# Optimization experiments

Hardware: AMD Instinct MI355X
Metric: run time of the kernel (lower is better)

## Reference

```python
import jax, jax.numpy as jnp
import numpy as np

B = 131072   # number of graphs (ranked lists)
G = 128      # candidates per graph
TEMPERATURE = 1.0

def setup_inputs() -> dict:
    key = jax.random.key(0)
    k1, k2 = jax.random.split(key)
    scores = jax.random.normal(k1, (B * G,), dtype=jnp.float32)
    labels = jax.random.randint(k2, (B * G,), 0, 2, dtype=jnp.int32)  # binary relevance
    batch = jnp.repeat(jnp.arange(B, dtype=jnp.int32), G)             # segment ids, sorted
    return {"scores": scores, "labels": labels, "batch": batch}

def reference(scores, labels, batch):
    # batch encodes B contiguous equal-size segments of length G; reshape replaces
    # the original per-graph Python loop with one vectorized pass.
    s = scores.reshape(B, G) / TEMPERATURE            # [B, G]
    l = labels.reshape(B, G).astype(s.dtype)          # [B, G]
    probs = jax.nn.softmax(s, axis=1)
    pos = jnp.arange(1, G + 1, dtype=s.dtype)
    disc = 1.0 / jnp.log2(pos + 1.0)                  # [G]
    expected_dcg = jnp.sum(probs * l * disc, axis=1)  # [B]
    sorted_l = -jnp.sort(-l, axis=1)                  # descending sort of labels
    idcg = jnp.sum(sorted_l * disc, axis=1)           # [B]
    valid = idcg > 0                                  # graphs with labels.sum()==0 contribute loss 0
    ndcg = expected_dcg / jnp.where(valid, idcg, 1.0)
    loss_g = jnp.where(valid, 1.0 - ndcg, 0.0)
    # original counts every non-NaN graph, including zero-label graphs -> divide by B
    return jnp.sum(loss_g) / B
```

## Files before the change

### kernel.cpp

```cpp
#include <hip/hip_runtime.h>
#include <math.h>


#define G 128

__global__ void build_cumdisc_kernel(float* __restrict__ cumdisc) {
    int t = threadIdx.x;
    if (t <= G) {
        float s = 0.0f;
        for (int p = 1; p <= t; ++p) {
            s += 1.0f / log2f((float)(p + 1));
        }
        cumdisc[t] = s;
    }
}

__global__ __launch_bounds__(256) void ndcg_main_kernel(
        const float* __restrict__ scores,
        const int*   __restrict__ labels,
        const float* __restrict__ cumdisc,
        float*       __restrict__ partials,
        int nquads) {
    const int lane = threadIdx.x & 63;
    const int li   = lane & 15;
    const int gs   = lane >> 4;
    const int waveInBlock = threadIdx.x >> 6;
    const int gwave  = blockIdx.x * (blockDim.x >> 6) + waveInBlock;
    const int nwaves = gridDim.x * (blockDim.x >> 6);

    float d[8];
#pragma unroll
    for (int j = 0; j < 8; ++j) {
        int p = li * 8 + j;
        d[j] = 1.0f / log2f((float)(p + 2));
    }

    float acc = 0.0f;
    for (int q = gwave; q < nquads; q += nwaves) {
        const long long g = (long long)q * 4 + gs;
        const float4* sp = (const float4*)(scores + g * G + li * 8);
        const int4*   lp = (const int4*)(labels + g * G + li * 8);
        float4 sA = sp[0], sB = sp[1];
        int4   lA = lp[0], lB = lp[1];

        float s[8] = {sA.x, sA.y, sA.z, sA.w, sB.x, sB.y, sB.z, sB.w};
        int   l[8] = {lA.x, lA.y, lA.z, lA.w, lB.x, lB.y, lB.z, lB.w};

        float esum = 0.0f, num = 0.0f;
        int cnt = 0;
#pragma unroll
        for (int j = 0; j < 8; ++j) {
            float e = __expf(s[j]);
            esum += e;
            num  += e * d[j] * (float)l[j];
            cnt  += l[j];
        }

        float cntf = (float)cnt;
#pragma unroll
        for (int m = 1; m <= 8; m <<= 1) {
            esum += __shfl_xor(esum, m, 64);
            num  += __shfl_xor(num,  m, 64);
            cntf += __shfl_xor(cntf, m, 64);
        }
        int c = (int)cntf;
        float idcg = cumdisc[c];
        float loss = (c > 0) ? (1.0f - num / (esum * idcg)) : 0.0f;
        if (li == 0) acc += loss;
    }

    __shared__ float red[256];
    red[threadIdx.x] = acc;
    __syncthreads();
    for (int s2 = 128; s2 > 0; s2 >>= 1) {
        if (threadIdx.x < s2) red[threadIdx.x] += red[threadIdx.x + s2];
        __syncthreads();
    }
    if (threadIdx.x == 0) partials[blockIdx.x] = red[0];
}

__global__ void finalize_kernel(const float* __restrict__ partials, int n,
                                float* __restrict__ out, float invB) {
    __shared__ float red[256];
    float a = 0.0f;
    for (int i = threadIdx.x; i < n; i += 256) a += partials[i];
    red[threadIdx.x] = a;
    __syncthreads();
    for (int s = 128; s > 0; s >>= 1) {
        if (threadIdx.x < s) red[threadIdx.x] += red[threadIdx.x + s];
        __syncthreads();
    }
    if (threadIdx.x == 0) out[0] = red[0] * invB;
}

extern "C" void kernel_launch(void* const* d_in, const int* in_sizes, int n_in,
                              void* d_out, int out_size, void* d_ws, size_t ws_size,
                              hipStream_t stream) {
    const float* scores = (const float*)d_in[0];
    const int*   labels = (const int*)d_in[1];

    const int n = in_sizes[0];
    const int B = n / G;
    const int nquads = B / 4;

    float* ws       = (float*)d_ws;
    float* partials = ws;
    float* cumdisc  = ws + 4096;

    const int NB = 2048;

    build_cumdisc_kernel<<<1, 256, 0, stream>>>(cumdisc);
    ndcg_main_kernel<<<NB, 256, 0, stream>>>(scores, labels, cumdisc, partials, nquads);
    finalize_kernel<<<1, 256, 0, stream>>>(partials, NB, (float*)d_out,
                                           1.0f / (float)B);
}
```

Baseline: 187.3 us.

## Map one wave to four graphs with a block per sixteen graphs

Drops the grid-stride loop. Each 256-thread block now handles exactly 16 graphs, giving B/16 = 8192 blocks, so each thread issues its loads once with no loop overhead. The per-thread log2 discount computation is replaced by a lookup table built in the setup kernel. The shared-memory tree reduction becomes wave shuffles plus a 4-entry sum. The cost is 4x more partials for the single-block finalize kernel to sum, and more block launch and scheduling overhead.

```diff
diff --git a/kernel.cpp b/kernel.cpp
--- a/kernel.cpp
+++ b/kernel.cpp
@@ -4,79 +4,69 @@
 
 #define G 128
 
-__global__ void build_cumdisc_kernel(float* __restrict__ cumdisc) {
+__global__ void build_tables_kernel(float* __restrict__ tabs) {
     int t = threadIdx.x;
+    if (t < G) {
+        tabs[t] = 1.0f / log2f((float)(t + 2));
+    }
     if (t <= G) {
         float s = 0.0f;
-        for (int p = 1; p <= t; ++p) {
-            s += 1.0f / log2f((float)(p + 1));
-        }
-        cumdisc[t] = s;
+        for (int p = 1; p <= t; ++p) s += 1.0f / log2f((float)(p + 1));
+        tabs[G + t] = s;
     }
 }
 
 __global__ __launch_bounds__(256) void ndcg_main_kernel(
         const float* __restrict__ scores,
         const int*   __restrict__ labels,
-        const float* __restrict__ cumdisc,
-        float*       __restrict__ partials,
-        int nquads) {
+        const float* __restrict__ tabs,
+        float*       __restrict__ partials) {
     const int lane = threadIdx.x & 63;
     const int li   = lane & 15;
-    const int gs   = lane >> 4;
-    const int waveInBlock = threadIdx.x >> 6;
-    const int gwave  = blockIdx.x * (blockDim.x >> 6) + waveInBlock;
-    const int nwaves = gridDim.x * (blockDim.x >> 6);
+    const int wib  = threadIdx.x >> 6;
+    const long long g = (long long)blockIdx.x * 16 + wib * 4 + (lane >> 4);
+    const long long base = g * G + li * 8;
 
-    float d[8];
+    const float4* sp = (const float4*)(scores + base);
+    const int4*   lp = (const int4*)(labels + base);
+    const float4* dp = (const float4*)(tabs + li * 8);
+    float4 sA = sp[0], sB = sp[1];
+    int4   lA = lp[0], lB = lp[1];
+    float4 dA = dp[0], dB = dp[1];
+
+    float s[8] = {sA.x, sA.y, sA.z, sA.w, sB.x, sB.y, sB.z, sB.w};
+    int   l[8] = {lA.x, lA.y, lA.z, lA.w, lB.x, lB.y, lB.z, lB.w};
+    float d[8] = {dA.x, dA.y, dA.z, dA.w, dB.x, dB.y, dB.z, dB.w};
+
+    float esum = 0.0f, num = 0.0f;
+    int cnt = 0;
 #pragma unroll
     for (int j = 0; j < 8; ++j) {
-        int p = li * 8 + j;
-        d[j] = 1.0f / log2f((float)(p + 2));
+        float e = __expf(s[j]);
+        esum += e;
+        num  += e * d[j] * (float)l[j];
+        cnt  += l[j];
     }
 
-    float acc = 0.0f;
-    for (int q = gwave; q < nquads; q += nwaves) {
-        const long long g = (long long)q * 4 + gs;
-        const float4* sp = (const float4*)(scores + g * G + li * 8);
-        const int4*   lp = (const int4*)(labels + g * G + li * 8);
-        float4 sA = sp[0], sB = sp[1];
-        int4   lA = lp[0], lB = lp[1];
+    float cntf = (float)cnt;
+#pragma unroll
+    for (int m = 1; m <= 8; m <<= 1) {
+        esum += __shfl_xor(esum, m, 64);
+        num  += __shfl_xor(num,  m, 64);
+        cntf += __shfl_xor(cntf, m, 64);
+    }
+    int c = (int)cntf;
+    float idcg = tabs[G + c];
+    float loss = (c > 0) ? (1.0f - num / (esum * idcg)) : 0.0f;
 
-        float s[8] = {sA.x, sA.y, sA.z, sA.w, sB.x, sB.y, sB.z, sB.w};
-        int   l[8] = {lA.x, lA.y, lA.z, lA.w, lB.x, lB.y, lB.z, lB.w};
+    loss += __shfl_xor(loss, 16, 64);
+    loss += __shfl_xor(loss, 32, 64);
 
-        float esum = 0.0f, num = 0.0f;
-        int cnt = 0;
-#pragma unroll
-        for (int j = 0; j < 8; ++j) {
-            float e = __expf(s[j]);
-            esum += e;
-            num  += e * d[j] * (float)l[j];
-            cnt  += l[j];
-        }
-
-        float cntf = (float)cnt;
-#pragma unroll
-        for (int m = 1; m <= 8; m <<= 1) {
-            esum += __shfl_xor(esum, m, 64);
-            num  += __shfl_xor(num,  m, 64);
-            cntf += __shfl_xor(cntf, m, 64);
-        }
-        int c = (int)cntf;
-        float idcg = cumdisc[c];
-        float loss = (c > 0) ? (1.0f - num / (esum * idcg)) : 0.0f;
-        if (li == 0) acc += loss;
-    }
-
-    __shared__ float red[256];
-    red[threadIdx.x] = acc;
+    __shared__ float wsum[4];
+    if (lane == 0) wsum[wib] = loss;
     __syncthreads();
-    for (int s2 = 128; s2 > 0; s2 >>= 1) {
-        if (threadIdx.x < s2) red[threadIdx.x] += red[threadIdx.x + s2];
-        __syncthreads();
-    }
-    if (threadIdx.x == 0) partials[blockIdx.x] = red[0];
+    if (threadIdx.x == 0)
+        partials[blockIdx.x] = wsum[0] + wsum[1] + wsum[2] + wsum[3];
 }
 
 __global__ void finalize_kernel(const float* __restrict__ partials, int n,
@@ -101,16 +91,13 @@
 
     const int n = in_sizes[0];
     const int B = n / G;
-    const int nquads = B / 4;
+    const int NB = B / 16;
 
-    float* ws       = (float*)d_ws;
-    float* partials = ws;
-    float* cumdisc  = ws + 4096;
+    float* tabs     = (float*)d_ws;
+    float* partials = tabs + 512;
 
-    const int NB = 2048;
-
-    build_cumdisc_kernel<<<1, 256, 0, stream>>>(cumdisc);
-    ndcg_main_kernel<<<NB, 256, 0, stream>>>(scores, labels, cumdisc, partials, nquads);
+    build_tables_kernel<<<1, 256, 0, stream>>>(tabs);
+    ndcg_main_kernel<<<NB, 256, 0, stream>>>(scores, labels, tabs, partials);
     finalize_kernel<<<1, 256, 0, stream>>>(partials, NB, (float*)d_out,
                                            1.0f / (float)B);
 }
```

Measured after the change: 190.0 us. About the same (+1.5%).
